# Performance work log

Hardware: AMD Instinct MI355X
Metric: run time of the kernel (lower is better)

Reference implementation:

```python
import jax, jax.numpy as jnp
import numpy as np

B, N, E = 64, 512, 8192          # graphs, nodes per graph, edges per graph
F_IN, H, C = 128, 128, 10        # in features, hidden, classes
K1, K2 = 256, 128                # dense pool cluster counts: ceil(.5*N), ceil(.5*K1)
EPS = 1e-15


def setup_inputs():
    key = jax.random.key(0)
    keys = jax.random.split(key, 32)
    it = iter(keys)
    def w(shape, fan_in):
        return jax.random.normal(next(it), shape, jnp.float32) / np.sqrt(fan_in)
    x = jax.random.normal(next(it), (B * N, F_IN), jnp.float32)
    src_l = jax.random.randint(next(it), (B, E), 0, N)
    dst_l = jax.random.randint(next(it), (B, E), 0, N)
    off = (jnp.arange(B) * N)[:, None]
    src = (src_l + off).reshape(-1).astype(jnp.int32)
    dst = (dst_l + off).reshape(-1).astype(jnp.int32)
    return dict(
        x=x, src=src, dst=dst,
        conv0_wr=w((F_IN, H), F_IN), conv0_wroot=w((F_IN, H), F_IN), conv0_b=jnp.zeros((H,), jnp.float32),
        sconv2_wr=w((H, H), H), sconv2_wroot=w((H, H), H), sconv2_b=jnp.zeros((H,), jnp.float32),
        sconv3_wr=w((H, H), H), sconv3_wroot=w((H, H), H), sconv3_b=jnp.zeros((H,), jnp.float32),
        sage1_wr=w((H, H), H), sage1_wroot=w((H, H), H), sage1_b=jnp.zeros((H,), jnp.float32),
        sage2_wr=w((H, H), H), sage2_wroot=w((H, H), H), sage2_b=jnp.zeros((H,), jnp.float32),
        pool0_w=w((H, K1), H), pool0_b=jnp.zeros((K1,), jnp.float32),
        pool1_w=w((H, K2), H), pool1_b=jnp.zeros((K2,), jnp.float32),
        p1=w((H,), H), p2=w((H,), H), p3=w((H,), H),
        lin1_1_w=w((2 * H, H), 2 * H), lin1_1_b=jnp.zeros((H,), jnp.float32),
        lin1_w=w((H, H), H), lin1_b=jnp.zeros((H,), jnp.float32),
        lin2_w=w((2 * H, C), 2 * H), lin2_b=jnp.zeros((C,), jnp.float32),
    )


def _graph_conv(x, src, dst, emask, wr, wroot, b, n):
    # PyG GraphConv: lin_rel(sum_j x_j) + lin_root(x_i); invalid edges masked to 0.
    msg = x[src] * emask[:, None]
    agg = jax.ops.segment_sum(msg, dst, num_segments=n)
    return agg @ wr + x @ wroot + b


def _topk_pool(x, score_w, src, dst, emask, n_per_graph, k):
    # TopK pooling (MPoolS): score = x.w/||w||, keep top ratio*n per graph, gate by tanh(score).
    score = x @ score_w / (jnp.linalg.norm(score_w) + 1e-16)
    idx = jax.lax.top_k(score.reshape(B, n_per_graph), k)[1]
    perm = (idx + (jnp.arange(B) * n_per_graph)[:, None]).reshape(-1)
    new_x = x[perm] * jnp.tanh(score[perm])[:, None]
    new_id = jnp.full((B * n_per_graph,), -1, jnp.int32).at[perm].set(
        jnp.arange(B * k, dtype=jnp.int32))
    ns, nd = new_id[src], new_id[dst]
    valid = (ns >= 0) & (nd >= 0) & (emask > 0)
    return new_x, jnp.where(valid, ns, 0), jnp.where(valid, nd, 0), valid.astype(x.dtype)


def _readout(x, k):
    # gmp || gap per graph (nodes are contiguous, k per graph)
    xr = x.reshape(B, k, -1)
    return jnp.concatenate([xr.max(axis=1), xr.mean(axis=1)], axis=-1)


def _dense_sage(x, adj, wr, wroot, b):
    agg = (adj @ x) / jnp.clip(adj.sum(-1, keepdims=True), 1.0, None)
    return agg @ wr + x @ wroot + b


def _dense_mincut_pool(x, adj, s):
    s = jax.nn.softmax(s, axis=-1)
    k = s.shape[-1]
    out = jnp.einsum('bnk,bnf->bkf', s, x)
    out_adj = jnp.einsum('bnk,bnm,bml->bkl', s, adj, s)
    mincut_num = jnp.trace(out_adj, axis1=-2, axis2=-1)
    deg = adj.sum(-1)
    mincut_den = jnp.einsum('bn,bnk,bnk->b', deg, s, s)
    mc = -jnp.mean(mincut_num / (mincut_den + EPS))
    ss = jnp.einsum('bnk,bnl->bkl', s, s)
    ss_n = jnp.linalg.norm(ss, axis=(1, 2), keepdims=True)
    eye = jnp.eye(k, dtype=x.dtype)
    o = jnp.mean(jnp.linalg.norm(ss / (ss_n + EPS) - eye / jnp.sqrt(k), axis=(1, 2)))
    di = jnp.arange(k)
    out_adj = out_adj.at[:, di, di].set(0.0)
    dpool = jnp.sqrt(out_adj.sum(-1)) + EPS
    out_adj = out_adj / dpool[:, :, None] / dpool[:, None, :]
    return out, out_adj, mc, o


def _forward(x, src, dst, conv0_wr, conv0_wroot, conv0_b, sconv2_wr, sconv2_wroot, sconv2_b,
             sconv3_wr, sconv3_wroot, sconv3_b, sage1_wr, sage1_wroot, sage1_b,
             sage2_wr, sage2_wroot, sage2_b, pool0_w, pool0_b, pool1_w, pool1_b,
             p1, p2, p3, lin1_1_w, lin1_1_b, lin1_w, lin1_b, lin2_w, lin2_b):
    relu = jax.nn.relu
    e0 = jnp.ones((src.shape[0],), x.dtype)
    x0 = relu(_graph_conv(x, src, dst, e0, conv0_wr, conv0_wroot, conv0_b, B * N))
    # ---- sparse (MPoolS / top-k) branch, stage 1 ----
    sx, s1, d1, m1 = _topk_pool(x0, p1, src, dst, e0, N, N // 2)
    sx1 = _readout(sx, N // 2)
    # ---- dense (DiffPool-style) branch ----
    xd = x0.reshape(B, N, H)                               # to_dense_batch (full mask)
    g = src // N
    adj = jnp.zeros((B, N, N), x.dtype).at[g, src % N, dst % N].add(1.0)  # to_dense_adj
    s = xd @ pool0_w + pool0_b
    xd, adj, mc, o = _dense_mincut_pool(xd, adj, s)
    xd = relu(_dense_sage(xd, adj, sage1_wr, sage1_wroot, sage1_b))
    s = xd @ pool1_w + pool1_b
    xd, adj, mc2, o2 = _dense_mincut_pool(xd, adj, s)
    mc, o = mc + mc2, o + o2
    xd = _dense_sage(xd, adj, sage2_wr, sage2_wroot, sage2_b)
    xg = relu(xd.mean(axis=1) @ lin1_w + lin1_b)
    # ---- sparse branch, stages 2 and 3 ----
    sx = relu(_graph_conv(sx, s1, d1, m1, sconv2_wr, sconv2_wroot, sconv2_b, B * (N // 2)))
    sx, s2, d2, m2 = _topk_pool(sx, p2, s1, d1, m1, N // 2, N // 4)
    sx2 = _readout(sx, N // 4)
    sx = relu(_graph_conv(sx, s2, d2, m2, sconv3_wr, sconv3_wroot, sconv3_b, B * (N // 4)))
    sx, s3, d3, m3 = _topk_pool(sx, p3, s2, d2, m2, N // 4, N // 8)
    sx3 = _readout(sx, N // 8)
    sxr = relu((sx1 + sx2 + sx3) @ lin1_1_w + lin1_1_b)
    logits = jnp.concatenate([sxr, xg], axis=-1) @ lin2_w + lin2_b
    return logits, mc, o


def reference(x, src, dst, conv0_wr, conv0_wroot, conv0_b, sconv2_wr, sconv2_wroot, sconv2_b,
              sconv3_wr, sconv3_wroot, sconv3_b, sage1_wr, sage1_wroot, sage1_b,
              sage2_wr, sage2_wroot, sage2_b, pool0_w, pool0_b, pool1_w, pool1_b,
              p1, p2, p3, lin1_1_w, lin1_1_b, lin1_w, lin1_b, lin2_w, lin2_b):
    return _forward(x, src, dst, conv0_wr, conv0_wroot, conv0_b, sconv2_wr, sconv2_wroot,
                    sconv2_b, sconv3_wr, sconv3_wroot, sconv3_b, sage1_wr, sage1_wroot,
                    sage1_b, sage2_wr, sage2_wroot, sage2_b, pool0_w, pool0_b, pool1_w,
                    pool1_b, p1, p2, p3, lin1_1_w, lin1_1_b, lin1_w, lin1_b, lin2_w, lin2_b)
```

## Files before the change

kernel.cpp:

```cpp
#include <hip/hip_runtime.h>
#include <math.h>

#define NGRAPH 64
#define NE 524288
#define EPG 8192
#define TSZ 2560

typedef short s16x8 __attribute__((ext_vector_type(8)));
typedef float f32x4 __attribute__((ext_vector_type(4)));

__device__ inline unsigned short f2bf(float f) {
    unsigned int u = __float_as_uint(f);
    return (unsigned short)((u + 0x7FFFu + ((u >> 16) & 1u)) >> 16);
}
__device__ inline float bf2f(unsigned short h) {
    return __uint_as_float((unsigned int)h << 16);
}
__device__ inline unsigned int f2pk(float v) {
    unsigned short h = f2bf(v);
    return (unsigned int)h | ((unsigned int)f2bf(v - bf2f(h)) << 16);
}
__device__ inline float pk2f(unsigned int u) {
    return __uint_as_float(u << 16) + __uint_as_float(u & 0xffff0000u);
}

__global__ void edge_count2(const int* __restrict__ keyA, int* __restrict__ cntA,
                            const int* __restrict__ keyB, int* __restrict__ cntB) {
    int e = blockIdx.x * 256 + threadIdx.x;
    if (e >= NE) return;
    if (blockIdx.y == 0) atomicAdd(&cntA[keyA[e]], 1);
    else                 atomicAdd(&cntB[keyB[e]], 1);
}

__device__ inline void scan_body(const int* __restrict__ counts, int* __restrict__ offs,
                                 int* __restrict__ cursor, int nPerGraph,
                                 float* __restrict__ degOut, int* s) {
    const int g = blockIdx.x, t = threadIdx.x;
    int v = (t < nPerGraph) ? counts[g * nPerGraph + t] : 0;
    s[t] = v; __syncthreads();
    for (int d = 1; d < 512; d <<= 1) {
        int u = (t >= d) ? s[t - d] : 0;
        __syncthreads();
        s[t] += u;
        __syncthreads();
    }
    if (t < nPerGraph) {
// ... 263 lines not shown
        }
        stageW_split(Wh, Wl, Kt, n0, k0, Bs, tid);
        __syncthreads();
        mfma_split(As, Bs, wm, wn, l15, quad, acc);
        __syncthreads();
    }
    #pragma unroll
    for (int mi = 0; mi < 2; ++mi)
    #pragma unroll
    for (int ni = 0; ni < 2; ++ni) {
        const int col = n0 + wn + (ni << 4) + l15;
        const float bv = bias ? bias[col] : 0.f;
        #pragma unroll
        for (int r = 0; r < 4; ++r) {
            const int row = m0 + wm + (mi << 4) + (quad << 2) + r;
            float v = acc[mi][ni][r] + bv;
            if (doRelu) v = fmaxf(v, 0.f);
            if (C)   C[(long long)row * Nn + col] = v;
            if (Cpk) Cpk[(long long)row * Nn + col] = f2pk(v);
        }
    }
}

__global__ __launch_bounds__(256) void gemm_tt(
    const unsigned int* __restrict__ Ap, const unsigned int* __restrict__ Bp,
    float* __restrict__ C, unsigned int* __restrict__ Cpk,
    float* __restrict__ fro,
    int Kd, int Mm, int Nn, int dual,
    long long sA, long long sB, long long sC)
{
    __shared__ short As[2 * TSZ], Bs[2 * TSZ], A2s[TSZ];
    __shared__ float redf[4];
    const int z = blockIdx.x;
    const unsigned int* Apz = Ap + (long long)z * sA;
    const unsigned int* Bpz = Bp + (long long)z * sB;
    const int m0 = blockIdx.y << 6, n0 = blockIdx.z << 6;
    const int tid = threadIdx.x, lane = tid & 63, wv = tid >> 6;
    const int l15 = lane & 15, quad = lane >> 4;
    const int wm = (wv & 1) << 5, wn = (wv >> 1) << 5;
    const int fw = dual ? ((m0 < n0) ? 2 : ((m0 == n0) ? 1 : 0)) : 0;
    f32x4 acc[2][2] = {};
    f32x4 accA[2][2] = {};
    for (int k0 = 0; k0 < Kd; k0 += 32) {
        stageT_pk(Apz, Mm, k0, m0, As, tid);
        stageT_pk(Bpz, Nn, k0, n0, Bs, tid);
        if (fw) stageT_hi_pk(Apz, Mm, k0, n0, A2s, tid);
        __syncthreads();
        mfma_split(As, Bs, wm, wn, l15, quad, acc);
        if (fw) mfma_hi(As, A2s, wm, wn, l15, quad, accA);
        __syncthreads();
    }
    float* Cp = C ? C + (long long)z * sC : nullptr;
    unsigned int* Ckp = Cpk ? Cpk + (long long)z * sC : nullptr;
    #pragma unroll
    for (int mi = 0; mi < 2; ++mi)
    #pragma unroll
    for (int ni = 0; ni < 2; ++ni) {
        const int col = n0 + wn + (ni << 4) + l15;
        #pragma unroll
        for (int r = 0; r < 4; ++r) {
            const int row = m0 + wm + (mi << 4) + (quad << 2) + r;
            const float v = acc[mi][ni][r];
            if (Cp)  Cp[(long long)row * Nn + col] = v;
            if (Ckp) Ckp[(long long)row * Nn + col] = f2pk(v);
        }
    }
    if (fw) {
        float s = 0.f;
        #pragma unroll
        for (int mi = 0; mi < 2; ++mi)
        #pragma unroll
        for (int ni = 0; ni < 2; ++ni)
        #pragma unroll
        for (int r = 0; r < 4; ++r) s += accA[mi][ni][r] * accA[mi][ni][r];
        s *= (float)fw;
        for (int off = 32; off; off >>= 1) s += __shfl_xor(s, off);
        if (lane == 0) redf[wv] = s;
        __syncthreads();
        if (tid == 0) atomicAdd(&fro[z], redf[0] + redf[1] + redf[2] + redf[3]);
    }
}

__global__ __launch_bounds__(256) void gemm_nt(
    const unsigned short* __restrict__ Ah, const unsigned short* __restrict__ Al,
    const unsigned int* __restrict__ Bp,
    float* __restrict__ C, unsigned int* __restrict__ Cpk,
    const float* __restrict__ rscale, int rsn,
    int Kd, int Nn, long long sA, long long sB, long long sC)
{
    __shared__ short As[2 * TSZ], Bs[2 * TSZ];
    const int z = blockIdx.x;
    const int m0 = blockIdx.y << 6, n0 = blockIdx.z << 6;
    const unsigned short* Aph = Ah + (long long)z * sA;
    const unsigned short* Apl = Al + (long long)z * sA;
    const unsigned int* Bpz = Bp + (long long)z * sB;
    const int tid = threadIdx.x, lane = tid & 63, wv = tid >> 6;
    const int l15 = lane & 15, quad = lane >> 4;
    const int wm = (wv & 1) << 5, wn = (wv >> 1) << 5;
    f32x4 acc[2][2] = {};
    for (int k0 = 0; k0 < Kd; k0 += 32) {
        stageW_split(Aph, Apl, Kd, m0, k0, As, tid);
        stageT_pk(Bpz, Nn, k0, n0, Bs, tid);
        __syncthreads();
        mfma_split(As, Bs, wm, wn, l15, quad, acc);
        __syncthreads();
    }
    #pragma unroll
    for (int mi = 0; mi < 2; ++mi)
    #pragma unroll
    for (int ni = 0; ni < 2; ++ni) {
        const int col = n0 + wn + (ni << 4) + l15;
        #pragma unroll
        for (int r = 0; r < 4; ++r) {
            const int row = m0 + wm + (mi << 4) + (quad << 2) + r;
            float v = acc[mi][ni][r];
            if (rscale) v *= rscale[z * rsn + row];
            if (C)   C[(long long)z * sC + (long long)row * Nn + col] = v;
            if (Cpk) Cpk[(long long)z * sC + (long long)row * Nn + col] = f2pk(v);
        }
    }
}

__global__ __launch_bounds__(256) void softmax_rows_wave(
    const float* __restrict__ sm, int L,
    const float* __restrict__ deg,
    float* __restrict__ rowq2, float* __restrict__ rowdq2, int totRows,
    unsigned int* __restrict__ opk)
{
    const int wid = (blockIdx.x * 256 + threadIdx.x) >> 6;
    const int lane = threadIdx.x & 63;
    if (wid >= totRows) return;
    const float* rowp = sm + (long long)wid * L;
    const int nv = L >> 6;
    float v[4];
    if (nv == 4) {
        float4 t = *(const float4*)&rowp[lane << 2];
        v[0] = t.x; v[1] = t.y; v[2] = t.z; v[3] = t.w;
    } else {
        float2 t = *(const float2*)&rowp[lane << 1];
        v[0] = t.x; v[1] = t.y;
    }
    float mx = v[0];
    for (int i = 1; i < nv; ++i) mx = fmaxf(mx, v[i]);
    for (int off = 32; off; off >>= 1) mx = fmaxf(mx, __shfl_xor(mx, off));
    float s = 0.f;
    for (int i = 0; i < nv; ++i) { v[i] = expf(v[i] - mx); s += v[i]; }
    for (int off = 32; off; off >>= 1) s += __shfl_xor(s, off);
    const float inv = 1.f / s;
    float q2 = 0.f;
    for (int i = 0; i < nv; ++i) { float p = v[i] * inv; v[i] = p; q2 += p * p; }
    const long long rb = (long long)wid * L;
    if (nv == 4) {
        uint4 pk;
        pk.x = f2pk(v[0]); pk.y = f2pk(v[1]); pk.z = f2pk(v[2]); pk.w = f2pk(v[3]);
        *(uint4*)&opk[rb + (lane << 2)] = pk;
    } else {
        uint2 pk;
        pk.x = f2pk(v[0]); pk.y = f2pk(v[1]);
        *(uint2*)&opk[rb + (lane << 1)] = pk;
    }
    for (int off = 32; off; off >>= 1) q2 += __shfl_xor(q2, off);
    if (lane == 0) { rowq2[wid] = q2; rowdq2[wid] = deg[wid] * q2; }
}

__global__ __launch_bounds__(256) void zdiag_rowsum_wave(
    float* __restrict__ adj, int K, float* __restrict__ dpool,
    float* __restrict__ rowdiag, int totRows)
{
    const int wid = (blockIdx.x * 256 + threadIdx.x) >> 6;
    const int lane = threadIdx.x & 63;
    if (wid >= totRows) return;
    const int b = wid / K;
    const int dcol = wid - b * K;
    float* rowp = adj + (long long)wid * K;
    const int nv = K >> 6;
    float s = 0.f, dval = 0.f;
    for (int q = 0; q < nv; ++q) {
        int c = lane + (q << 6);
        float v = rowp[c];
        if (c == dcol) { dval = v; rowp[c] = 0.f; v = 0.f; }
        s += v;
    }
    for (int off = 32; off; off >>= 1) s += __shfl_xor(s, off);
    if (lane == (dcol & 63)) rowdiag[wid] = dval;
    if (lane == 0) dpool[wid] = sqrtf(s) + 1e-15f;
}

__global__ __launch_bounds__(256) void norm_adj_wave(
    const float* __restrict__ adj, int K, const float* __restrict__ dpool,
    float* __restrict__ rowsum, float* __restrict__ rscale,
    unsigned short* __restrict__ oh, unsigned short* __restrict__ ol, int totRows)
{
    const int wid = (blockIdx.x * 256 + threadIdx.x) >> 6;
    const int lane = threadIdx.x & 63;
    if (wid >= totRows) return;
    const int b = wid / K;
    const float* rowp = adj + (long long)wid * K;
    const float inv_r = 1.f / dpool[wid];
    const int nv = K >> 6;
    float s = 0.f;
    for (int q = 0; q < nv; ++q) {
        int c = lane + (q << 6);
        float v = rowp[c] * inv_r / dpool[b * K + c];
        s += v;
        unsigned short h = f2bf(v);
        oh[(long long)wid * K + c] = h;
        ol[(long long)wid * K + c] = f2bf(v - bf2f(h));
    }
    for (int off = 32; off; off >>= 1) s += __shfl_xor(s, off);
    if (lane == 0) { rowsum[wid] = s; rscale[wid] = 1.f / fmaxf(s, 1.f); }
}

__global__ __launch_bounds__(256) void reduce2_pergraph(
    const float* __restrict__ a, const float* __restrict__ b, int rowsPerGraph,
    float* __restrict__ outA, float* __restrict__ outB)
{
    __shared__ float redA[4], redB[4];
    const int g = blockIdx.x, t = threadIdx.x;
    float sa = 0.f, sb = 0.f;
    for (int i = t; i < rowsPerGraph; i += 256) {
        sa += a[g * rowsPerGraph + i];
        if (b) sb += b[g * rowsPerGraph + i];
    }
    for (int off = 32; off; off >>= 1) { sa += __shfl_xor(sa, off); sb += __shfl_xor(sb, off); }
    const int wv = t >> 6;
    if ((t & 63) == 0) { redA[wv] = sa; redB[wv] = sb; }
    __syncthreads();
    if (t == 0) {
        outA[g] = redA[0] + redA[1] + redA[2] + redA[3];
        if (outB) outB[g] = redB[0] + redB[1] + redB[2] + redB[3];
    }
}

__global__ __launch_bounds__(512) void topk_kernel(
    const float* __restrict__ x, const float* __restrict__ p, int n, int k,
    int* __restrict__ new_id, int* __restrict__ sel, float* __restrict__ gate)
{
    __shared__ float sc[512];
    __shared__ int pref[512];
    const int g = blockIdx.x, tid = threadIdx.x;
    float myScore = 0.f;
    if (tid < n) {
        const float* xr = x + (long long)(g * n + tid) * 128;
        float pn2 = 0.f, d = 0.f;
        #pragma unroll 4
        for (int f = 0; f < 128; f += 4) {
            float4 pv = *(const float4*)&p[f];
            float4 v = *(const float4*)&xr[f];
            pn2 += pv.x * pv.x + pv.y * pv.y + pv.z * pv.z + pv.w * pv.w;
            d += v.x * pv.x + v.y * pv.y + v.z * pv.z + v.w * pv.w;
        }
        myScore = d / (sqrtf(pn2) + 1e-16f);
        sc[tid] = myScore;
    }
    __syncthreads();
    int keep = 0;
    if (tid < n) {
        const float si = myScore;
        int rank = 0;
        for (int j = 0; j < n; j += 4) {
            float4 s4 = *(const float4*)&sc[j];
            rank += (s4.x > si) || (s4.x == si && (j + 0) < tid);
            rank += (s4.y > si) || (s4.y == si && (j + 1) < tid);
            rank += (s4.z > si) || (s4.z == si && (j + 2) < tid);
            rank += (s4.w > si) || (s4.w == si && (j + 3) < tid);
        }
        keep = rank < k;
    }
    pref[tid] = keep;
    __syncthreads();
    for (int d = 1; d < 512; d <<= 1) {
        int u = (tid >= d) ? pref[tid - d] : 0;
        __syncthreads();
        pref[tid] += u;
        __syncthreads();
    }
    if (tid < n) {
        if (keep) {
            int pos = pref[tid] - 1;
            new_id[g * n + tid] = g * k + pos;
            sel[g * k + pos] = g * n + tid;
            gate[g * k + pos] = tanhf(myScore);
        } else new_id[g * n + tid] = -1;
    }
}

__global__ void gather_gate(const float* __restrict__ x, const int* __restrict__ sel,
                            const float* __restrict__ gate, float* __restrict__ out, int rows) {
    int t = blockIdx.x * blockDim.x + threadIdx.x;
    int r = t >> 5, q = (t & 31) << 2;
    if (r >= rows) return;
    float4 v = *(const float4*)&x[(long long)sel[r] * 128 + q];
    float gt = gate[r];
    v.x *= gt; v.y *= gt; v.z *= gt; v.w *= gt;
    *(float4*)&out[(long long)r * 128 + q] = v;
}

__global__ void remap_edges_count(const int* __restrict__ s, const int* __restrict__ d,
                                  const float* __restrict__ m, const int* __restrict__ new_id,
                                  int* __restrict__ so, int* __restrict__ do_,
                                  float* __restrict__ mo, int* __restrict__ counts) {
    int e = blockIdx.x * blockDim.x + threadIdx.x;
    if (e >= NE) return;
    int ns = new_id[s[e]], nd = new_id[d[e]];
    bool v = (ns >= 0) && (nd >= 0) && (m ? (m[e] > 0.f) : true);
    so[e] = v ? ns : 0; do_[e] = v ? nd : 0; mo[e] = v ? 1.f : 0.f;
    if (v) atomicAdd(&counts[nd], 1);
}

__global__ void readout_part(const float* __restrict__ x, int k,
                             float* __restrict__ pmax, float* __restrict__ psum) {
    int g = blockIdx.x, seg = blockIdx.y, f = threadIdx.x;
    int per = k >> 2;
    int r0 = seg * per;
    float mx0 = -INFINITY, mx1 = -INFINITY, sm0 = 0.f, sm1 = 0.f;
    int r = r0;
    for (; r + 2 <= r0 + per; r += 2) {
        float v0 = x[(long long)(g * k + r) * 128 + f];
        float v1 = x[(long long)(g * k + r + 1) * 128 + f];
        mx0 = fmaxf(mx0, v0); sm0 += v0;
        mx1 = fmaxf(mx1, v1); sm1 += v1;
    }
    for (; r < r0 + per; ++r) { float v = x[(long long)(g * k + r) * 128 + f]; mx0 = fmaxf(mx0, v); sm0 += v; }
    pmax[(g * 4 + seg) * 128 + f] = fmaxf(mx0, mx1);
    psum[(g * 4 + seg) * 128 + f] = sm0 + sm1;
}

__global__ void readout_comb(const float* __restrict__ pmax, const float* __restrict__ psum,
                             int k, float* __restrict__ sxsum) {
    int g = blockIdx.x, f = threadIdx.x;
    float mx = -INFINITY, sm = 0.f;
    #pragma unroll
    for (int s = 0; s < 4; ++s) {
        mx = fmaxf(mx, pmax[(g * 4 + s) * 128 + f]);
        sm += psum[(g * 4 + s) * 128 + f];
    }
    sxsum[g * 256 + f] += mx;
    sxsum[g * 256 + 128 + f] += sm / k;
}

__global__ void mean_lin(const float* __restrict__ xd, const float* __restrict__ W,
                         const float* __restrict__ bias, float* __restrict__ xg, int nNodes) {
    __shared__ float meanv[128];
    int b = blockIdx.x, t = threadIdx.x;
    float s = 0.f;
    for (int n = 0; n < nNodes; n++) s += xd[(long long)(b * nNodes + n) * 128 + t];
    meanv[t] = s / nNodes; __syncthreads();
    float acc = bias[t];
    for (int i = 0; i < 128; i++) acc += meanv[i] * W[i * 128 + t];
    xg[b * 128 + t] = fmaxf(acc, 0.f);
}

__global__ void final_head(const float* __restrict__ sxsum, const float* __restrict__ w11,
                           const float* __restrict__ b11, const float* __restrict__ xg,
                           const float* __restrict__ w2, const float* __restrict__ b2,
                           const float* __restrict__ accs, float* __restrict__ out) {
    __shared__ float sin_[256];
    __shared__ float cat[256];
    __shared__ float rm[2], ro[2];
    int b = blockIdx.x, t = threadIdx.x;
    if (b == 0) {
        int wvi = t >> 6, lane = t & 63;
        const float* acc = accs + wvi * 256;
        float sqrtk = wvi ? sqrtf(128.f) : 16.f;
        float numv = acc[lane], denv = acc[64 + lane], trv = acc[128 + lane], frov = acc[192 + lane];
        float mcb = numv / (denv + 1e-15f);
        float ssn = sqrtf(frov) + 1e-15f;
        float ob = sqrtf(fmaxf(frov / (ssn * ssn) - 2.f * trv / (ssn * sqrtk) + 1.f, 0.f));
        for (int off = 32; off; off >>= 1) { mcb += __shfl_down(mcb, off); ob += __shfl_down(ob, off); }
        if (lane == 0) { rm[wvi] = mcb; ro[wvi] = ob; }
        __syncthreads();
        if (t == 0) {
            out[640] = -(rm[0] + rm[1]) / 64.f;
            out[641] = (ro[0] + ro[1]) / 64.f;
        }
    }
    sin_[t] = sxsum[b * 256 + t];
    sin_[t + 128] = sxsum[b * 256 + 128 + t];
    __syncthreads();
    float acc = b11[t];
    for (int i = 0; i < 256; i++) acc += sin_[i] * w11[i * 128 + t];
    cat[t] = fmaxf(acc, 0.f);
    cat[128 + t] = xg[b * 128 + t];
    __syncthreads();
    if (t < 10) {
        float a = b2[t];
        for (int i = 0; i < 256; i++) a += cat[i] * w2[i * 10 + t];
        out[b * 10 + t] = a;
    }
}

extern "C" void kernel_launch(void* const* d_in, const int* in_sizes, int n_in,
                              void* d_out, int out_size, void* d_ws, size_t ws_size,
                              hipStream_t stream) {
    const float* x         = (const float*)d_in[0];
    const int*   src       = (const int*)d_in[1];
    const int*   dst       = (const int*)d_in[2];
    const float* conv0_wr  = (const float*)d_in[3];
    const float* conv0_wrt = (const float*)d_in[4];
    const float* conv0_b   = (const float*)d_in[5];
    const float* sc2_wr    = (const float*)d_in[6];
    const float* sc2_wrt   = (const float*)d_in[7];
    const float* sc2_b     = (const float*)d_in[8];
    const float* sc3_wr    = (const float*)d_in[9];
    const float* sc3_wrt   = (const float*)d_in[10];
    const float* sc3_b     = (const float*)d_in[11];
// ... 12 lines not shown
    const float* p3        = (const float*)d_in[24];
    const float* l11_w     = (const float*)d_in[25];
    const float* l11_b     = (const float*)d_in[26];
    const float* l1_w      = (const float*)d_in[27];
    const float* l1_b      = (const float*)d_in[28];
    const float* l2_w      = (const float*)d_in[29];
    const float* l2_b      = (const float*)d_in[30];
    float* out = (float*)d_out;

    char* w = (char*)d_ws;
    const unsigned long long MBy = 1ull << 20;
    float* x0    = (float*)(w + 0);
    float* BIG1  = (float*)(w + 16 * MBy);
    float* BIG2  = (float*)(w + 48 * MBy);
    float* agg   = (float*)(w + 80 * MBy);
    float* adj1  = (float*)(w + 104 * MBy);
    int*   s1    = (int*)(w + 120 * MBy);
    int*   d1    = (int*)(w + 122 * MBy);
    float* m1    = (float*)(w + 124 * MBy);
    int*   s2e   = (int*)(w + 126 * MBy);
    int*   d2e   = (int*)(w + 128 * MBy);
    float* m2e   = (float*)(w + 130 * MBy);
    char*  misc  = w + 132 * MBy;
    float* score = (float*)(misc);
    int*   sel   = (int*)(misc + 128 * 1024);
    float* gate  = (float*)(misc + 192 * 1024);
    int*   newid = (int*)(misc + 256 * 1024);
    float* deg   = (float*)(misc + 384 * 1024);
    float* dpool = (float*)(misc + 512 * 1024);
    float* rowsum2 = (float*)(misc + 576 * 1024);
    float* rscale2 = (float*)(misc + 640 * 1024);
    float* dpool2  = (float*)(misc + 704 * 1024);
    float* rowsum3 = (float*)(misc + 736 * 1024);
    float* rscale3 = (float*)(misc + 768 * 1024);
    float* accs    = (float*)(misc + 800 * 1024);
    float* sxsum   = (float*)(misc + 900 * 1024);
    float* xg      = (float*)(misc + 964 * 1024);

    unsigned short* wt_sg1h   = (unsigned short*)(misc + 1024 * 1024);
    unsigned short* wt_sg1l   = wt_sg1h + 32768;
    unsigned short* wt_sg2h   = wt_sg1l + 32768;
    unsigned short* wt_sg2l   = wt_sg2h + 32768;
    unsigned short* wt_pool0h = wt_sg2l + 32768;
    unsigned short* wt_pool0l = wt_pool0h + 32768;
    unsigned short* wt_pool1h = wt_pool0l + 32768;
    unsigned short* wt_pool1l = wt_pool1h + 32768;
    unsigned short* wt_c0h    = wt_pool1l + 32768;
    unsigned short* wt_c0l    = wt_c0h + 32768;
    unsigned short* wt_sc2h   = wt_c0l + 32768;
    unsigned short* wt_sc2l   = wt_sc2h + 32768;
    unsigned short* wt_sc3h   = wt_sc2l + 32768;
    unsigned short* wt_sc3l   = wt_sc3h + 32768;

    float* pmax = (float*)(misc + 2048 * 1024);
    float* psum = pmax + 32768;

    float* rowq2  = score;
    float* rowdq2 = (float*)newid;
    float* rowdiag = (float*)sel;

    float* s_sm  = BIG1;
    unsigned int* Tbp = (unsigned int*)BIG2;
    float* s2sm  = BIG2 + 4 * 1024 * 1024;
    unsigned int* T2p = (unsigned int*)((char*)BIG2 + 24 * MBy);
    float* outx2 = BIG1;
    float* adj2b = BIG1 + 1024 * 1024;
    float* xd2   = BIG1 + 2 * 1024 * 1024;
    float* sxA   = BIG1 + 3 * 1024 * 1024;
    float* sxE   = BIG1 + 5 * 1024 * 1024;
    float* sxB   = x0;
    float* sxC   = x0 + 2 * 1024 * 1024;
    float* sxD   = x0 + 3 * 1024 * 1024;

    unsigned int* s_smp = (unsigned int*)(w + 136 * MBy);
    unsigned int* x0p   = (unsigned int*)(w + 168 * MBy);
    unsigned int* ox1p  = (unsigned int*)(w + 184 * MBy);
    unsigned int* xd1p  = (unsigned int*)(w + 192 * MBy);
    unsigned int* s2p   = (unsigned int*)(w + 200 * MBy);
    unsigned int* ox2p  = (unsigned int*)(w + 208 * MBy);
    unsigned short* a1h = (unsigned short*)(w + 212 * MBy);
    unsigned short* a1l = (unsigned short*)(w + 220 * MBy);
    unsigned short* a2h = (unsigned short*)(w + 228 * MBy);
    unsigned short* a2l = (unsigned short*)(w + 230 * MBy);
    unsigned int* AXp   = (unsigned int*)(w + 232 * MBy);
    unsigned int* AXp2  = (unsigned int*)(w + 240 * MBy);

    unsigned int* aggp  = (unsigned int*)agg;
    unsigned int* agg2p = (unsigned int*)agg;
// ... 23 lines not shown
    hipMemsetAsync(cntA, 0, 65536 * sizeof(int), stream);

    {
        WSpec a{sg1_wr, sg1_wrt, 128, 128, 128, wt_sg1h, wt_sg1l};
        WSpec b{sg2_wr, sg2_wrt, 128, 128, 128, wt_sg2h, wt_sg2l};
        WSpec c{pool0_w, nullptr, 128, 0, 256, wt_pool0h, wt_pool0l};
        WSpec d{pool1_w, nullptr, 128, 0, 128, wt_pool1h, wt_pool1l};
        WSpec e{conv0_wr, conv0_wrt, 128, 128, 128, wt_c0h, wt_c0l};
        WSpec f{sc2_wr, sc2_wrt, 128, 128, 128, wt_sc2h, wt_sc2l};
        WSpec g{sc3_wr, sc3_wrt, 128, 128, 128, wt_sc3h, wt_sc3l};
        wconv_all<<<dim3(128, 7), 256, 0, stream>>>(a, b, c, d, e, f, g);
    }

    edge_count2<<<dim3(2048, 2), 256, 0, stream>>>(dst, cntA, src, cntB);
    scan_offsets2<<<dim3(64, 2), 512, 0, stream>>>(cntA, offA, curA, cntB, offB, curB, 512, deg);
    edge_fill2<<<dim3(2048, 2), 256, 0, stream>>>(dst, src, curA, elA, src, dst, curB, elB);

    gather_csr<<<4096, 256, 0, stream>>>(x, nullptr, 128, offA, cntA, elA, aggp, 32768, 512);
    gemm_aw<<<dim3(2, 512), 256, 0, stream>>>(aggp, nullptr, 128, nullptr, x, 128,
        wt_c0h, wt_c0l, conv0_b, x0, x0p, 128, 1);

    gemm_aw<<<dim3(4, 512), 256, 0, stream>>>(x0p, nullptr, 128, nullptr, nullptr, 0,
        wt_pool0h, wt_pool0l, pool0_b, s_sm, nullptr, 256, 0);
    softmax_rows_wave<<<8192, 256, 0, stream>>>(s_sm, 256, deg, rowq2, rowdq2, 32768, s_smp);
    reduce2_pergraph<<<64, 256, 0, stream>>>(rowq2, rowdq2, 512, accs + 128, accs + 64);
    gather_csr<<<8192, 256, 0, stream>>>(nullptr, s_smp, 256, offB, cntB, elB, Tbp, 32768, 512);
    gemm_tt<<<dim3(64, 4, 2), 256, 0, stream>>>(s_smp, x0p, nullptr, ox1p,
        nullptr, 512, 256, 128, 0, 512 * 256, 512 * 128, 256 * 128);
    gemm_tt<<<dim3(64, 4, 4), 256, 0, stream>>>(s_smp, Tbp, adj1, nullptr,
        accs + 192, 512, 256, 256, 1, 512 * 256, 512 * 256, 256 * 256);
    zdiag_rowsum_wave<<<4096, 256, 0, stream>>>(adj1, 256, dpool, rowdiag, 16384);
    reduce2_pergraph<<<64, 256, 0, stream>>>(rowdiag, nullptr, 256, accs + 0, nullptr);
    norm_adj_wave<<<4096, 256, 0, stream>>>(adj1, 256, dpool, rowsum2, rscale2, a1h, a1l, 16384);
    gemm_nt<<<dim3(64, 4, 2), 256, 0, stream>>>(a1h, a1l, ox1p, nullptr, AXp, rscale2, 256,
        256, 128, 256 * 256, 256 * 128, 256 * 128);
    gemm_aw<<<dim3(2, 256), 256, 0, stream>>>(AXp, nullptr, 128, ox1p, nullptr, 128,
        wt_sg1h, wt_sg1l, sg1_b, nullptr, xd1p, 128, 1);
    gemm_aw<<<dim3(2, 256), 256, 0, stream>>>(xd1p, nullptr, 128, nullptr, nullptr, 0,
        wt_pool1h, wt_pool1l, pool1_b, s2sm, nullptr, 128, 0);
    softmax_rows_wave<<<4096, 256, 0, stream>>>(s2sm, 128, rowsum2, rowq2, rowdq2, 16384, s2p);
    reduce2_pergraph<<<64, 256, 0, stream>>>(rowq2, rowdq2, 256, accs + 384, accs + 320);
    gemm_nt<<<dim3(64, 4, 2), 256, 0, stream>>>(a1h, a1l, s2p, nullptr, T2p, nullptr, 0,
        256, 128, 256 * 256, 256 * 128, 256 * 128);
    gemm_tt<<<dim3(64, 2, 2), 256, 0, stream>>>(s2p, xd1p, nullptr, ox2p,
        nullptr, 256, 128, 128, 0, 256 * 128, 256 * 128, 128 * 128);
    gemm_tt<<<dim3(64, 2, 2), 256, 0, stream>>>(s2p, T2p, adj2b, nullptr,
        accs + 448, 256, 128, 128, 1, 256 * 128, 256 * 128, 128 * 128);
    zdiag_rowsum_wave<<<2048, 256, 0, stream>>>(adj2b, 128, dpool2, rowdiag, 8192);
    reduce2_pergraph<<<64, 256, 0, stream>>>(rowdiag, nullptr, 128, accs + 256, nullptr);
    norm_adj_wave<<<2048, 256, 0, stream>>>(adj2b, 128, dpool2, rowsum3, rscale3, a2h, a2l, 8192);
    gemm_nt<<<dim3(64, 2, 2), 256, 0, stream>>>(a2h, a2l, ox2p, nullptr, AXp2, rscale3, 128,
        128, 128, 128 * 128, 128 * 128, 128 * 128);
    gemm_aw<<<dim3(2, 128), 256, 0, stream>>>(AXp2, nullptr, 128, ox2p, nullptr, 128,
        wt_sg2h, wt_sg2l, sg2_b, xd2, nullptr, 128, 0);
    mean_lin<<<64, 128, 0, stream>>>(xd2, l1_w, l1_b, xg, 128);

    topk_kernel<<<64, 512, 0, stream>>>(x0, p1, 512, 256, newid, sel, gate);
    gather_gate<<<2048, 256, 0, stream>>>(x0, sel, gate, sxA, 16384);
    hipMemsetAsync(cntC, 0, 16384 * sizeof(int), stream);
    remap_edges_count<<<2048, 256, 0, stream>>>(src, dst, nullptr, newid, s1, d1, m1, cntC);
    readout_part<<<dim3(64, 4), 128, 0, stream>>>(sxA, 256, pmax, psum);
    readout_comb<<<64, 128, 0, stream>>>(pmax, psum, 256, sxsum);
    scan_offsets<<<64, 512, 0, stream>>>(cntC, offC, curC, 256, nullptr);
    edge_fill<<<2048, 256, 0, stream>>>(d1, s1, m1, curC, elC);
    gather_csr<<<2048, 256, 0, stream>>>(sxA, nullptr, 128, offC, cntC, elC, agg2p, 16384, 256);
    gemm_aw<<<dim3(2, 256), 256, 0, stream>>>(agg2p, nullptr, 128, nullptr, sxA, 128,
        wt_sc2h, wt_sc2l, sc2_b, sxB, nullptr, 128, 1);
    topk_kernel<<<64, 512, 0, stream>>>(sxB, p2, 256, 128, newid, sel, gate);
    gather_gate<<<1024, 256, 0, stream>>>(sxB, sel, gate, sxC, 8192);
    hipMemsetAsync(cntD, 0, 8192 * sizeof(int), stream);
    remap_edges_count<<<2048, 256, 0, stream>>>(s1, d1, m1, newid, s2e, d2e, m2e, cntD);
    readout_part<<<dim3(64, 4), 128, 0, stream>>>(sxC, 128, pmax, psum);
    readout_comb<<<64, 128, 0, stream>>>(pmax, psum, 128, sxsum);
    scan_offsets<<<64, 512, 0, stream>>>(cntD, offD, curD, 128, nullptr);
    edge_fill<<<2048, 256, 0, stream>>>(d2e, s2e, m2e, curD, elD);
    gather_csr<<<1024, 256, 0, stream>>>(sxC, nullptr, 128, offD, cntD, elD, agg3p, 8192, 128);
    gemm_aw<<<dim3(2, 128), 256, 0, stream>>>(agg3p, nullptr, 128, nullptr, sxC, 128,
        wt_sc3h, wt_sc3l, sc3_b, sxD, nullptr, 128, 1);
    topk_kernel<<<64, 512, 0, stream>>>(sxD, p3, 128, 64, newid, sel, gate);
    gather_gate<<<512, 256, 0, stream>>>(sxD, sel, gate, sxE, 4096);
    readout_part<<<dim3(64, 4), 128, 0, stream>>>(sxE, 64, pmax, psum);
    readout_comb<<<64, 128, 0, stream>>>(pmax, psum, 64, sxsum);

    final_head<<<64, 128, 0, stream>>>(sxsum, l11_w, l11_b, xg, l2_w, l2_b, accs, out);
}
```

Measured before the change: 667.4 us.

## Fuse small post-processing kernels and merge paired gemm_tt launches

Several chains of small launches are collapsed. The two gemm_tt calls that share an A operand now run as one launch, with blockIdx.z picking between two parameter sets. The diag/rowsum and normalize passes are merged into a single per-graph adjnorm kernel. Topk, gather_gate, readout and the count memset are combined into topk_fused, and mean_lin is folded into final_head. Softmax per-row reductions now go straight into per-graph accumulators through atomics instead of a separate reduce pass. The aim is to cut launch count and intermediate traffic. The cost is that adjnorm runs only 64 blocks, which may underfill the GPU, and the float atomics change summation order.

New measurement: 1.028 ms. +54.0%, slower.

```diff
diff --git a/kernel.cpp b/kernel.cpp
--- a/kernel.cpp
+++ b/kernel.cpp
@@ -19,9 +19,6 @@
 __device__ inline unsigned int f2pk(float v) {
     unsigned short h = f2bf(v);
     return (unsigned int)h | ((unsigned int)f2bf(v - bf2f(h)) << 16);
-}
-__device__ inline float pk2f(unsigned int u) {
-    return __uint_as_float(u << 16) + __uint_as_float(u & 0xffff0000u);
 }
 
 __global__ void edge_count2(const int* __restrict__ keyA, int* __restrict__ cntA,
@@ -331,36 +328,43 @@
     }
 }
 
+struct TTSet {
+    const unsigned int* Bp;
+    float* C; unsigned int* Cpk; float* fro;
+    int Nn; int dual;
+    long long sB, sC;
+};
+
 __global__ __launch_bounds__(256) void gemm_tt(
-    const unsigned int* __restrict__ Ap, const unsigned int* __restrict__ Bp,
-    float* __restrict__ C, unsigned int* __restrict__ Cpk,
-    float* __restrict__ fro,
-    int Kd, int Mm, int Nn, int dual,
-    long long sA, long long sB, long long sC)
+    const unsigned int* __restrict__ Ap, int Kd, int Mm, long long sA,
+    int zsplit, TTSet t0, TTSet t1)
 {
     __shared__ short As[2 * TSZ], Bs[2 * TSZ], A2s[TSZ];
     __shared__ float redf[4];
     const int z = blockIdx.x;
+    int nz = blockIdx.z;
+    const TTSet tt = (nz < zsplit) ? t0 : t1;
+    if (blockIdx.z >= zsplit) nz -= zsplit;
     const unsigned int* Apz = Ap + (long long)z * sA;
-    const unsigned int* Bpz = Bp + (long long)z * sB;
-    const int m0 = blockIdx.y << 6, n0 = blockIdx.z << 6;
+    const unsigned int* Bpz = tt.Bp + (long long)z * tt.sB;
+    const int m0 = blockIdx.y << 6, n0 = nz << 6;
     const int tid = threadIdx.x, lane = tid & 63, wv = tid >> 6;
     const int l15 = lane & 15, quad = lane >> 4;
     const int wm = (wv & 1) << 5, wn = (wv >> 1) << 5;
-    const int fw = dual ? ((m0 < n0) ? 2 : ((m0 == n0) ? 1 : 0)) : 0;
+    const int fw = tt.dual ? ((m0 < n0) ? 2 : ((m0 == n0) ? 1 : 0)) : 0;
     f32x4 acc[2][2] = {};
     f32x4 accA[2][2] = {};
     for (int k0 = 0; k0 < Kd; k0 += 32) {
         stageT_pk(Apz, Mm, k0, m0, As, tid);
-        stageT_pk(Bpz, Nn, k0, n0, Bs, tid);
+        stageT_pk(Bpz, tt.Nn, k0, n0, Bs, tid);
         if (fw) stageT_hi_pk(Apz, Mm, k0, n0, A2s, tid);
         __syncthreads();
         mfma_split(As, Bs, wm, wn, l15, quad, acc);
         if (fw) mfma_hi(As, A2s, wm, wn, l15, quad, accA);
         __syncthreads();
     }
-    float* Cp = C ? C + (long long)z * sC : nullptr;
-    unsigned int* Ckp = Cpk ? Cpk + (long long)z * sC : nullptr;
+    float* Cp = tt.C ? tt.C + (long long)z * tt.sC : nullptr;
+    unsigned int* Ckp = tt.Cpk ? tt.Cpk + (long long)z * tt.sC : nullptr;
     #pragma unroll
     for (int mi = 0; mi < 2; ++mi)
     #pragma unroll
@@ -370,8 +374,8 @@
         for (int r = 0; r < 4; ++r) {
             const int row = m0 + wm + (mi << 4) + (quad << 2) + r;
             const float v = acc[mi][ni][r];
-            if (Cp)  Cp[(long long)row * Nn + col] = v;
-            if (Ckp) Ckp[(long long)row * Nn + col] = f2pk(v);
+            if (Cp)  Cp[(long long)row * tt.Nn + col] = v;
+            if (Ckp) Ckp[(long long)row * tt.Nn + col] = f2pk(v);
         }
     }
     if (fw) {
@@ -386,7 +390,7 @@
         for (int off = 32; off; off >>= 1) s += __shfl_xor(s, off);
         if (lane == 0) redf[wv] = s;
         __syncthreads();
-        if (tid == 0) atomicAdd(&fro[z], redf[0] + redf[1] + redf[2] + redf[3]);
+        if (tid == 0) atomicAdd(&tt.fro[z], redf[0] + redf[1] + redf[2] + redf[3]);
     }
 }
 
@@ -433,7 +437,8 @@
 __global__ __launch_bounds__(256) void softmax_rows_wave(
     const float* __restrict__ sm, int L,
     const float* __restrict__ deg,
-    float* __restrict__ rowq2, float* __restrict__ rowdq2, int totRows,
+    float* __restrict__ accQ, float* __restrict__ accD,
+    int rowsPerGraph, int totRows,
     unsigned int* __restrict__ opk)
 {
     const int wid = (blockIdx.x * 256 + threadIdx.x) >> 6;
@@ -469,85 +474,78 @@
         *(uint2*)&opk[rb + (lane << 1)] = pk;
     }
     for (int off = 32; off; off >>= 1) q2 += __shfl_xor(q2, off);
-    if (lane == 0) { rowq2[wid] = q2; rowdq2[wid] = deg[wid] * q2; }
-}
-
-__global__ __launch_bounds__(256) void zdiag_rowsum_wave(
-    float* __restrict__ adj, int K, float* __restrict__ dpool,
-    float* __restrict__ rowdiag, int totRows)
+    if (lane == 0) {
+        const int g = wid / rowsPerGraph;
+        atomicAdd(&accQ[g], q2);
+        atomicAdd(&accD[g], deg[wid] * q2);
+    }
+}
+
+__global__ __launch_bounds__(1024) void adjnorm(
+    const float* __restrict__ adj, int K,
+    float* __restrict__ trace_out,
+    float* __restrict__ rowsum, float* __restrict__ rscale,
+    unsigned short* __restrict__ oh, unsigned short* __restrict__ ol)
 {
-    const int wid = (blockIdx.x * 256 + threadIdx.x) >> 6;
-    const int lane = threadIdx.x & 63;
-    if (wid >= totRows) return;
-    const int b = wid / K;
-    const int dcol = wid - b * K;
-    float* rowp = adj + (long long)wid * K;
+    __shared__ float dpoolL[256];
+    __shared__ float trL;
+    const int g = blockIdx.x, tid = threadIdx.x;
+    const int wv = tid >> 6, lane = tid & 63;
+    if (tid == 0) trL = 0.f;
+    __syncthreads();
+    const int rowsPerWave = K >> 4;
     const int nv = K >> 6;
-    float s = 0.f, dval = 0.f;
-    for (int q = 0; q < nv; ++q) {
-        int c = lane + (q << 6);
-        float v = rowp[c];
-        if (c == dcol) { dval = v; rowp[c] = 0.f; v = 0.f; }
-        s += v;
-    }
-    for (int off = 32; off; off >>= 1) s += __shfl_xor(s, off);
-    if (lane == (dcol & 63)) rowdiag[wid] = dval;
-    if (lane == 0) dpool[wid] = sqrtf(s) + 1e-15f;
-}
-
-__global__ __launch_bounds__(256) void norm_adj_wave(
-    const float* __restrict__ adj, int K, const float* __restrict__ dpool,
-    float* __restrict__ rowsum, float* __restrict__ rscale,
-    unsigned short* __restrict__ oh, unsigned short* __restrict__ ol, int totRows)
-{
-    const int wid = (blockIdx.x * 256 + threadIdx.x) >> 6;
-    const int lane = threadIdx.x & 63;
-    if (wid >= totRows) return;
-    const int b = wid / K;
-    const float* rowp = adj + (long long)wid * K;
-    const float inv_r = 1.f / dpool[wid];
-    const int nv = K >> 6;
-    float s = 0.f;
-    for (int q = 0; q < nv; ++q) {
-        int c = lane + (q << 6);
-        float v = rowp[c] * inv_r / dpool[b * K + c];
-        s += v;
-        unsigned short h = f2bf(v);
-        oh[(long long)wid * K + c] = h;
-        ol[(long long)wid * K + c] = f2bf(v - bf2f(h));
-    }
-    for (int off = 32; off; off >>= 1) s += __shfl_xor(s, off);
-    if (lane == 0) { rowsum[wid] = s; rscale[wid] = 1.f / fmaxf(s, 1.f); }
-}
-
-__global__ __launch_bounds__(256) void reduce2_pergraph(
-    const float* __restrict__ a, const float* __restrict__ b, int rowsPerGraph,
-    float* __restrict__ outA, float* __restrict__ outB)
-{
-    __shared__ float redA[4], redB[4];
-    const int g = blockIdx.x, t = threadIdx.x;
-    float sa = 0.f, sb = 0.f;
-    for (int i = t; i < rowsPerGraph; i += 256) {
-        sa += a[g * rowsPerGraph + i];
-        if (b) sb += b[g * rowsPerGraph + i];
-    }
-    for (int off = 32; off; off >>= 1) { sa += __shfl_xor(sa, off); sb += __shfl_xor(sb, off); }
-    const int wv = t >> 6;
-    if ((t & 63) == 0) { redA[wv] = sa; redB[wv] = sb; }
+    float trpart = 0.f;
+    for (int rr = 0; rr < rowsPerWave; ++rr) {
+        const int r = wv * rowsPerWave + rr;
+        const float* rowp = adj + (long long)(g * K + r) * K;
+        float s = 0.f, dval = 0.f;
+        for (int q = 0; q < nv; ++q) {
+            int c = lane + (q << 6);
+            float v = rowp[c];
+            if (c == r) { dval = v; v = 0.f; }
+            s += v;
+        }
+        for (int off = 32; off; off >>= 1) s += __shfl_xor(s, off);
+        for (int off = 32; off; off >>= 1) dval += __shfl_xor(dval, off);
+        if (lane == 0) { dpoolL[r] = sqrtf(s) + 1e-15f; trpart += dval; }
+    }
+    if (lane == 0) atomicAdd(&trL, trpart);
     __syncthreads();
-    if (t == 0) {
-        outA[g] = redA[0] + redA[1] + redA[2] + redA[3];
-        if (outB) outB[g] = redB[0] + redB[1] + redB[2] + redB[3];
-    }
-}
-
-__global__ __launch_bounds__(512) void topk_kernel(
+    if (tid == 0) trace_out[g] = trL;
+    for (int rr = 0; rr < rowsPerWave; ++rr) {
+        const int r = wv * rowsPerWave + rr;
+        const int wid = g * K + r;
+        const float* rowp = adj + (long long)wid * K;
+        const float inv_r = 1.f / dpoolL[r];
+        float s = 0.f;
+        for (int q = 0; q < nv; ++q) {
+            int c = lane + (q << 6);
+            float a = rowp[c];
+            if (c == r) a = 0.f;
+            float v = a * inv_r / dpoolL[c];
+            s += v;
+            unsigned short h = f2bf(v);
+            oh[(long long)wid * K + c] = h;
+            ol[(long long)wid * K + c] = f2bf(v - bf2f(h));
+        }
+        for (int off = 32; off; off >>= 1) s += __shfl_xor(s, off);
+        if (lane == 0) { rowsum[wid] = s; rscale[wid] = 1.f / fmaxf(s, 1.f); }
+    }
+}
+
+__global__ __launch_bounds__(512) void topk_fused(
     const float* __restrict__ x, const float* __restrict__ p, int n, int k,
-    int* __restrict__ new_id, int* __restrict__ sel, float* __restrict__ gate)
+    int* __restrict__ new_id, float* __restrict__ outx,
+    float* __restrict__ sxsum, int* __restrict__ cntZero)
 {
     __shared__ float sc[512];
     __shared__ int pref[512];
+    __shared__ int   selL[256];
+    __shared__ float gateL[256];
+    __shared__ float red[1024];
     const int g = blockIdx.x, tid = threadIdx.x;
+    if (cntZero && tid < k) cntZero[g * k + tid] = 0;
     float myScore = 0.f;
     if (tid < n) {
         const float* xr = x + (long long)(g * n + tid) * 128;
@@ -588,21 +586,27 @@
         if (keep) {
             int pos = pref[tid] - 1;
             new_id[g * n + tid] = g * k + pos;
-            sel[g * k + pos] = g * n + tid;
-            gate[g * k + pos] = tanhf(myScore);
+            selL[pos] = g * n + tid;
+            gateL[pos] = tanhf(myScore);
         } else new_id[g * n + tid] = -1;
     }
-}
-
-__global__ void gather_gate(const float* __restrict__ x, const int* __restrict__ sel,
-                            const float* __restrict__ gate, float* __restrict__ out, int rows) {
-    int t = blockIdx.x * blockDim.x + threadIdx.x;
-    int r = t >> 5, q = (t & 31) << 2;
-    if (r >= rows) return;
-    float4 v = *(const float4*)&x[(long long)sel[r] * 128 + q];
-    float gt = gate[r];
-    v.x *= gt; v.y *= gt; v.z *= gt; v.w *= gt;
-    *(float4*)&out[(long long)r * 128 + q] = v;
+    __syncthreads();
+    const int f = tid & 127, grp = tid >> 7;
+    float mx = -INFINITY, sm = 0.f;
+    for (int r = grp; r < k; r += 4) {
+        float v = x[(long long)selL[r] * 128 + f] * gateL[r];
+        outx[(long long)(g * k + r) * 128 + f] = v;
+        mx = fmaxf(mx, v); sm += v;
+    }
+    red[grp * 128 + f] = mx;
+    red[512 + grp * 128 + f] = sm;
+    __syncthreads();
+    if (tid < 128) {
+        float m = fmaxf(fmaxf(red[f], red[128 + f]), fmaxf(red[256 + f], red[384 + f]));
+        float s2 = red[512 + f] + red[640 + f] + red[768 + f] + red[896 + f];
+        sxsum[g * 256 + f] += m;
+        sxsum[g * 256 + 128 + f] += s2 / k;
+    }
 }
 
 __global__ void remap_edges_count(const int* __restrict__ s, const int* __restrict__ d,
@@ -617,57 +621,22 @@
     if (v) atomicAdd(&counts[nd], 1);
 }
 
-__global__ void readout_part(const float* __restrict__ x, int k,
-                             float* __restrict__ pmax, float* __restrict__ psum) {
-    int g = blockIdx.x, seg = blockIdx.y, f = threadIdx.x;
-    int per = k >> 2;
-    int r0 = seg * per;
-    float mx0 = -INFINITY, mx1 = -INFINITY, sm0 = 0.f, sm1 = 0.f;
-    int r = r0;
-    for (; r + 2 <= r0 + per; r += 2) {
-        float v0 = x[(long long)(g * k + r) * 128 + f];
-        float v1 = x[(long long)(g * k + r + 1) * 128 + f];
-        mx0 = fmaxf(mx0, v0); sm0 += v0;
-        mx1 = fmaxf(mx1, v1); sm1 += v1;
-    }
-    for (; r < r0 + per; ++r) { float v = x[(long long)(g * k + r) * 128 + f]; mx0 = fmaxf(mx0, v); sm0 += v; }
-    pmax[(g * 4 + seg) * 128 + f] = fmaxf(mx0, mx1);
-    psum[(g * 4 + seg) * 128 + f] = sm0 + sm1;
-}
-
-__global__ void readout_comb(const float* __restrict__ pmax, const float* __restrict__ psum,
-                             int k, float* __restrict__ sxsum) {
-    int g = blockIdx.x, f = threadIdx.x;
-    float mx = -INFINITY, sm = 0.f;
-    #pragma unroll
-    for (int s = 0; s < 4; ++s) {
-        mx = fmaxf(mx, pmax[(g * 4 + s) * 128 + f]);
-        sm += psum[(g * 4 + s) * 128 + f];
-    }
-    sxsum[g * 256 + f] += mx;
-    sxsum[g * 256 + 128 + f] += sm / k;
-}
-
-__global__ void mean_lin(const float* __restrict__ xd, const float* __restrict__ W,
-                         const float* __restrict__ bias, float* __restrict__ xg, int nNodes) {
-    __shared__ float meanv[128];
-    int b = blockIdx.x, t = threadIdx.x;
-    float s = 0.f;
-    for (int n = 0; n < nNodes; n++) s += xd[(long long)(b * nNodes + n) * 128 + t];
-    meanv[t] = s / nNodes; __syncthreads();
-    float acc = bias[t];
-    for (int i = 0; i < 128; i++) acc += meanv[i] * W[i * 128 + t];
-    xg[b * 128 + t] = fmaxf(acc, 0.f);
-}
-
 __global__ void final_head(const float* __restrict__ sxsum, const float* __restrict__ w11,
-                           const float* __restrict__ b11, const float* __restrict__ xg,
+                           const float* __restrict__ b11,
+                           const float* __restrict__ xd2, const float* __restrict__ l1w,
+                           const float* __restrict__ l1b,
                            const float* __restrict__ w2, const float* __restrict__ b2,
                            const float* __restrict__ accs, float* __restrict__ out) {
+    __shared__ float meanv[128];
     __shared__ float sin_[256];
     __shared__ float cat[256];
     __shared__ float rm[2], ro[2];
     int b = blockIdx.x, t = threadIdx.x;
+    {
+        float s = 0.f;
+        for (int n = 0; n < 128; n++) s += xd2[(long long)(b * 128 + n) * 128 + t];
+        meanv[t] = s / 128.f;
+    }
     if (b == 0) {
         int wvi = t >> 6, lane = t & 63;
         const float* acc = accs + wvi * 256;
@@ -690,7 +659,9 @@
     float acc = b11[t];
     for (int i = 0; i < 256; i++) acc += sin_[i] * w11[i * 128 + t];
     cat[t] = fmaxf(acc, 0.f);
-    cat[128 + t] = xg[b * 128 + t];
+    float xga = l1b[t];
+    for (int i = 0; i < 128; i++) xga += meanv[i] * l1w[i * 128 + t];
+    cat[128 + t] = fmaxf(xga, 0.f);
     __syncthreads();
     if (t < 10) {
         float a = b2[t];
@@ -749,20 +720,14 @@
     int*   d2e   = (int*)(w + 128 * MBy);
     float* m2e   = (float*)(w + 130 * MBy);
     char*  misc  = w + 132 * MBy;
-    float* score = (float*)(misc);
-    int*   sel   = (int*)(misc + 128 * 1024);
-    float* gate  = (float*)(misc + 192 * 1024);
     int*   newid = (int*)(misc + 256 * 1024);
     float* deg   = (float*)(misc + 384 * 1024);
-    float* dpool = (float*)(misc + 512 * 1024);
     float* rowsum2 = (float*)(misc + 576 * 1024);
     float* rscale2 = (float*)(misc + 640 * 1024);
-    float* dpool2  = (float*)(misc + 704 * 1024);
     float* rowsum3 = (float*)(misc + 736 * 1024);
     float* rscale3 = (float*)(misc + 768 * 1024);
     float* accs    = (float*)(misc + 800 * 1024);
     float* sxsum   = (float*)(misc + 900 * 1024);
-    float* xg      = (float*)(misc + 964 * 1024);
 
     unsigned short* wt_sg1h   = (unsigned short*)(misc + 1024 * 1024);
     unsigned short* wt_sg1l   = wt_sg1h + 32768;
@@ -779,18 +744,10 @@
     unsigned short* wt_sc3h   = wt_sc2l + 32768;
     unsigned short* wt_sc3l   = wt_sc3h + 32768;
 
-    float* pmax = (float*)(misc + 2048 * 1024);
-    float* psum = pmax + 32768;
-
-    float* rowq2  = score;
-    float* rowdq2 = (float*)newid;
-    float* rowdiag = (float*)sel;
-
     float* s_sm  = BIG1;
     unsigned int* Tbp = (unsigned int*)BIG2;
     float* s2sm  = BIG2 + 4 * 1024 * 1024;
     unsigned int* T2p = (unsigned int*)((char*)BIG2 + 24 * MBy);
-    float* outx2 = BIG1;
     float* adj2b = BIG1 + 1024 * 1024;
     float* xd2   = BIG1 + 2 * 1024 * 1024;
     float* sxA   = BIG1 + 3 * 1024 * 1024;
@@ -860,65 +817,52 @@
 
     gemm_aw<<<dim3(4, 512), 256, 0, stream>>>(x0p, nullptr, 128, nullptr, nullptr, 0,
         wt_pool0h, wt_pool0l, pool0_b, s_sm, nullptr, 256, 0);
-    softmax_rows_wave<<<8192, 256, 0, stream>>>(s_sm, 256, deg, rowq2, rowdq2, 32768, s_smp);
-    reduce2_pergraph<<<64, 256, 0, stream>>>(rowq2, rowdq2, 512, accs + 128, accs + 64);
+    softmax_rows_wave<<<8192, 256, 0, stream>>>(s_sm, 256, deg, accs + 128, accs + 64,
+        512, 32768, s_smp);
     gather_csr<<<8192, 256, 0, stream>>>(nullptr, s_smp, 256, offB, cntB, elB, Tbp, 32768, 512);
-    gemm_tt<<<dim3(64, 4, 2), 256, 0, stream>>>(s_smp, x0p, nullptr, ox1p,
-        nullptr, 512, 256, 128, 0, 512 * 256, 512 * 128, 256 * 128);
-    gemm_tt<<<dim3(64, 4, 4), 256, 0, stream>>>(s_smp, Tbp, adj1, nullptr,
-        accs + 192, 512, 256, 256, 1, 512 * 256, 512 * 256, 256 * 256);
-    zdiag_rowsum_wave<<<4096, 256, 0, stream>>>(adj1, 256, dpool, rowdiag, 16384);
-    reduce2_pergraph<<<64, 256, 0, stream>>>(rowdiag, nullptr, 256, accs + 0, nullptr);
-    norm_adj_wave<<<4096, 256, 0, stream>>>(adj1, 256, dpool, rowsum2, rscale2, a1h, a1l, 16384);
+    {
+        TTSet t0{x0p, nullptr, ox1p, nullptr, 128, 0, 512 * 128, 256 * 128};
+        TTSet t1{Tbp, adj1, nullptr, accs + 192, 256, 1, 512 * 256, 256 * 256};
+        gemm_tt<<<dim3(64, 4, 6), 256, 0, stream>>>(s_smp, 512, 256, 512 * 256, 2, t0, t1);
+    }
+    adjnorm<<<64, 1024, 0, stream>>>(adj1, 256, accs + 0, rowsum2, rscale2, a1h, a1l);
     gemm_nt<<<dim3(64, 4, 2), 256, 0, stream>>>(a1h, a1l, ox1p, nullptr, AXp, rscale2, 256,
         256, 128, 256 * 256, 256 * 128, 256 * 128);
     gemm_aw<<<dim3(2, 256), 256, 0, stream>>>(AXp, nullptr, 128, ox1p, nullptr, 128,
         wt_sg1h, wt_sg1l, sg1_b, nullptr, xd1p, 128, 1);
     gemm_aw<<<dim3(2, 256), 256, 0, stream>>>(xd1p, nullptr, 128, nullptr, nullptr, 0,
         wt_pool1h, wt_pool1l, pool1_b, s2sm, nullptr, 128, 0);
-    softmax_rows_wave<<<4096, 256, 0, stream>>>(s2sm, 128, rowsum2, rowq2, rowdq2, 16384, s2p);
-    reduce2_pergraph<<<64, 256, 0, stream>>>(rowq2, rowdq2, 256, accs + 384, accs + 320);
+    softmax_rows_wave<<<4096, 256, 0, stream>>>(s2sm, 128, rowsum2, accs + 384, accs + 320,
+        256, 16384, s2p);
     gemm_nt<<<dim3(64, 4, 2), 256, 0, stream>>>(a1h, a1l, s2p, nullptr, T2p, nullptr, 0,
         256, 128, 256 * 256, 256 * 128, 256 * 128);
-    gemm_tt<<<dim3(64, 2, 2), 256, 0, stream>>>(s2p, xd1p, nullptr, ox2p,
-        nullptr, 256, 128, 128, 0, 256 * 128, 256 * 128, 128 * 128);
-    gemm_tt<<<dim3(64, 2, 2), 256, 0, stream>>>(s2p, T2p, adj2b, nullptr,
-        accs + 448, 256, 128, 128, 1, 256 * 128, 256 * 128, 128 * 128);
-    zdiag_rowsum_wave<<<2048, 256, 0, stream>>>(adj2b, 128, dpool2, rowdiag, 8192);
-    reduce2_pergraph<<<64, 256, 0, stream>>>(rowdiag, nullptr, 128, accs + 256, nullptr);
-    norm_adj_wave<<<2048, 256, 0, stream>>>(adj2b, 128, dpool2, rowsum3, rscale3, a2h, a2l, 8192);
+    {
+        TTSet t0{xd1p, nullptr, ox2p, nullptr, 128, 0, 256 * 128, 128 * 128};
+        TTSet t1{T2p, adj2b, nullptr, accs + 448, 128, 1, 256 * 128, 128 * 128};
+        gemm_tt<<<dim3(64, 2, 4), 256, 0, stream>>>(s2p, 256, 128, 256 * 128, 2, t0, t1);
+    }
+    adjnorm<<<64, 1024, 0, stream>>>(adj2b, 128, accs + 256, rowsum3, rscale3, a2h, a2l);
     gemm_nt<<<dim3(64, 2, 2), 256, 0, stream>>>(a2h, a2l, ox2p, nullptr, AXp2, rscale3, 128,
         128, 128, 128 * 128, 128 * 128, 128 * 128);
     gemm_aw<<<dim3(2, 128), 256, 0, stream>>>(AXp2, nullptr, 128, ox2p, nullptr, 128,
         wt_sg2h, wt_sg2l, sg2_b, xd2, nullptr, 128, 0);
-    mean_lin<<<64, 128, 0, stream>>>(xd2, l1_w, l1_b, xg, 128);
-
-    topk_kernel<<<64, 512, 0, stream>>>(x0, p1, 512, 256, newid, sel, gate);
-    gather_gate<<<2048, 256, 0, stream>>>(x0, sel, gate, sxA, 16384);
-    hipMemsetAsync(cntC, 0, 16384 * sizeof(int), stream);
+
+    topk_fused<<<64, 512, 0, stream>>>(x0, p1, 512, 256, newid, sxA, sxsum, cntC);
     remap_edges_count<<<2048, 256, 0, stream>>>(src, dst, nullptr, newid, s1, d1, m1, cntC);
-    readout_part<<<dim3(64, 4), 128, 0, stream>>>(sxA, 256, pmax, psum);
-    readout_comb<<<64, 128, 0, stream>>>(pmax, psum, 256, sxsum);
     scan_offsets<<<64, 512, 0, stream>>>(cntC, offC, curC, 256, nullptr);
     edge_fill<<<2048, 256, 0, stream>>>(d1, s1, m1, curC, elC);
     gather_csr<<<2048, 256, 0, stream>>>(sxA, nullptr, 128, offC, cntC, elC, agg2p, 16384, 256);
     gemm_aw<<<dim3(2, 256), 256, 0, stream>>>(agg2p, nullptr, 128, nullptr, sxA, 128,
         wt_sc2h, wt_sc2l, sc2_b, sxB, nullptr, 128, 1);
-    topk_kernel<<<64, 512, 0, stream>>>(sxB, p2, 256, 128, newid, sel, gate);
-    gather_gate<<<1024, 256, 0, stream>>>(sxB, sel, gate, sxC, 8192);
-    hipMemsetAsync(cntD, 0, 8192 * sizeof(int), stream);
+    topk_fused<<<64, 512, 0, stream>>>(sxB, p2, 256, 128, newid, sxC, sxsum, cntD);
     remap_edges_count<<<2048, 256, 0, stream>>>(s1, d1, m1, newid, s2e, d2e, m2e, cntD);
-    readout_part<<<dim3(64, 4), 128, 0, stream>>>(sxC, 128, pmax, psum);
-    readout_comb<<<64, 128, 0, stream>>>(pmax, psum, 128, sxsum);
     scan_offsets<<<64, 512, 0, stream>>>(cntD, offD, curD, 128, nullptr);
     edge_fill<<<2048, 256, 0, stream>>>(d2e, s2e, m2e, curD, elD);
     gather_csr<<<1024, 256, 0, stream>>>(sxC, nullptr, 128, offD, cntD, elD, agg3p, 8192, 128);
     gemm_aw<<<dim3(2, 128), 256, 0, stream>>>(agg3p, nullptr, 128, nullptr, sxC, 128,
         wt_sc3h, wt_sc3l, sc3_b, sxD, nullptr, 128, 1);
-    topk_kernel<<<64, 512, 0, stream>>>(sxD, p3, 128, 64, newid, sel, gate);
-    gather_gate<<<512, 256, 0, stream>>>(sxD, sel, gate, sxE, 4096);
-    readout_part<<<dim3(64, 4), 128, 0, stream>>>(sxE, 64, pmax, psum);
-    readout_comb<<<64, 128, 0, stream>>>(pmax, psum, 64, sxsum);
-
-    final_head<<<64, 128, 0, stream>>>(sxsum, l11_w, l11_b, xg, l2_w, l2_b, accs, out);
-}
+    topk_fused<<<64, 512, 0, stream>>>(sxD, p3, 128, 64, newid, sxE, sxsum, nullptr);
+
+    final_head<<<64, 128, 0, stream>>>(sxsum, l11_w, l11_b, xd2, l1_w, l1_b,
+        l2_w, l2_b, accs, out);
+}
```
